# Performance work log

Measured on AMD Instinct MI355X. Metric: run time of the kernel, lower is better.

The kernel has to match this reference:

```python
import jax, jax.numpy as jnp
import numpy as np

P = 64          # num_populations
T = 8192        # buffer_size (buffer assumed full / all valid)
K = 8           # num_bins
HIST = 2        # history_length
NPAST = K ** HIST          # number of single-series past states
NCOMB = NPAST * NPAST      # joint (y_past, x_past) states
N = T - HIST - 1           # n_samples per pair


def _discretize(x):
    # Faithful to torch _discretize: min-max normalize, floor into K bins.
    xmin = x.min()
    xmax = x.max()
    rng = xmax - xmin
    norm = (x - xmin) / (rng + 1e-8)
    b = jnp.clip((norm * (K - 1)).astype(jnp.int32), 0, K - 1)
    return jnp.where(rng < 1e-8, jnp.zeros_like(b), b)


def _cond_entropy(counts, state_mask):
    # counts: (S, K) histogram of y_future per conditioning state.
    # Torch skips states with total count < 2; weight = count/N.
    tot = counts.sum(axis=1)                          # (S,)
    valid = (tot >= 2.0) & state_mask
    p = counts / jnp.maximum(tot[:, None], 1.0)
    p_safe = jnp.where(counts > 0, p, 1.0)
    h = -jnp.where(counts > 0, p * jnp.log2(p_safe), 0.0).sum(axis=1)
    w = tot / N
    return jnp.where(valid, w * h, 0.0).sum()


def _te(src_d, tgt_d):
    # src_d, tgt_d: (T,) int bins. TE(src -> tgt) in bits.
    yf = tgt_d[HIST + 1: HIST + 1 + N]                # y_future, (N,)
    # hash of k-step histories: sum_i K**i * series[k-i : k-i+N]
    yp = sum((K ** i) * tgt_d[HIST - i: HIST - i + N] for i in range(HIST))
    xp = sum((K ** i) * src_d[HIST - i: HIST - i + N] for i in range(HIST))
    # joint histograms via scatter-add (the fused histogram kernel target)
    cy = jnp.zeros((NPAST, K), jnp.float32).at[yp, yf].add(1.0)
    cc = jnp.zeros((NCOMB, K), jnp.float32).at[yp * NPAST + xp, yf].add(1.0)
    # torch loops yp in range(min(NPAST, N)) -> mask out higher state ids
    mask_y = jnp.arange(NPAST) < min(NPAST, N)
    h_y_given_yp = _cond_entropy(cy, mask_y)
    h_y_given_ypxp = _cond_entropy(cc, jnp.ones((NCOMB,), dtype=bool))
    return jnp.maximum(0.0, h_y_given_yp - h_y_given_ypxp)


def setup_inputs() -> dict:
    key = jax.random.key(0)
    return {"time_series": jax.random.normal(key, (T, P), dtype=jnp.float32)}


def reference(time_series):
    # time_series: (T, P). Returns flow_matrix (P, P): flow[i, j] = TE(i -> j).
    d = jax.vmap(_discretize, in_axes=1, out_axes=0)(time_series)  # (P, T) int
    flow = jax.vmap(lambda s: jax.vmap(lambda t: _te(s, t))(d))(d)  # (P, P)
    return flow * (1.0 - jnp.eye(P, dtype=flow.dtype))  # diagonal forced to 0
```

## Files before the change

kernel.cpp:

```cpp
#include <hip/hip_runtime.h>

static constexpr int T = 8192;
static constexpr int P = 64;
static constexpr int NSAMP = 8189;

__global__ __launch_bounds__(1024) void prep_kernel(const float* __restrict__ ts,
        unsigned short* __restrict__ A, unsigned short* __restrict__ X,
        float* __restrict__ h_y)
{
    __shared__ float col[T];
    __shared__ unsigned char bins[T];
    __shared__ unsigned int cy[512];
    __shared__ float wred[32];
    const int p = blockIdx.x, tid = threadIdx.x;
    const int lane = tid & 63, wave = tid >> 6;

    float mn = 3.402823466e38f, mx = -3.402823466e38f;
    for (int t = tid; t < T; t += 1024) {
        float v = ts[t * P + p];
        col[t] = v;
        mn = fminf(mn, v);
        mx = fmaxf(mx, v);
    }
    #pragma unroll
    for (int off = 32; off > 0; off >>= 1) {
        mn = fminf(mn, __shfl_down(mn, off, 64));
        mx = fmaxf(mx, __shfl_down(mx, off, 64));
    }
    if (lane == 0) { wred[wave] = mn; wred[16 + wave] = mx; }
    for (int i = tid; i < 512; i += 1024) cy[i] = 0u;
    __syncthreads();
    float xmin = wred[0], xmax = wred[16];
    #pragma unroll
    for (int j = 1; j < 16; ++j) {
        xmin = fminf(xmin, wred[j]);
        xmax = fmaxf(xmax, wred[16 + j]);
    }
    const float rng = xmax - xmin;
    const float den = rng + 1e-8f;
    const int flat = rng < 1e-8f;

    for (int t = tid; t < T; t += 1024) {
        float norm = (col[t] - xmin) / den;
        int b = (int)(norm * 7.0f);
        b = b < 0 ? 0 : (b > 7 ? 7 : b);
        bins[t] = flat ? (unsigned char)0 : (unsigned char)b;
    }
    __syncthreads();

    unsigned short* Ap = A + p * T;
    unsigned short* Xp = X + p * T;
    for (int i = tid * 4; i + 3 < NSAMP; i += 4096) {
        unsigned w0 = *(const unsigned*)&bins[i];
        unsigned w1 = *(const unsigned*)&bins[i + 4];
        unsigned long long bb = (unsigned long long)w0 | ((unsigned long long)w1 << 32);
        ushort4 av, xv;
        unsigned short* ap = (unsigned short*)&av;
        unsigned short* xp = (unsigned short*)&xv;
        #pragma unroll
        for (int j = 0; j < 4; ++j) {
            unsigned b1 = (unsigned)(bb >> (8 * (j + 1))) & 255u;
            unsigned b2 = (unsigned)(bb >> (8 * (j + 2))) & 255u;
            unsigned b3 = (unsigned)(bb >> (8 * (j + 3))) & 255u;
            unsigned yp = b2 + 8u * b1;
            ap[j] = (unsigned short)(yp * 512u + b3);
            xp[j] = (unsigned short)(yp * 8u);
            atomicAdd(&cy[yp * 8u + b3], 1u);
        }
        *(ushort4*)(Ap + i) = av;
        *(ushort4*)(Xp + i) = xv;
    }
    if (tid == 0) {
        unsigned b1 = bins[NSAMP], b2 = bins[NSAMP + 1], b3 = bins[NSAMP + 2];
        unsigned yp = b2 + 8u * b1;
        Ap[NSAMP - 1] = (unsigned short)(yp * 512u + b3);
        Xp[NSAMP - 1] = (unsigned short)(yp * 8u);
        atomicAdd(&cy[yp * 8u + b3], 1u);
    }
    __syncthreads();

    if (tid < 64) {
        float tot = 0.0f, sc = 0.0f;
        #pragma unroll
        for (int v = 0; v < 8; ++v) {
            unsigned c = cy[tid * 8 + v];
            if (c) { float fc = (float)c; tot += fc; sc += fc * log2f(fc); }
        }
        float acc = (tot >= 2.0f) ? (tot * log2f(tot) - sc) : 0.0f;
        #pragma unroll
        for (int off = 32; off > 0; off >>= 1) acc += __shfl_down(acc, off, 64);
        if (tid == 0) h_y[p] = acc * (1.0f / (float)NSAMP);
    }
}

__global__ __launch_bounds__(256) void pair_kernel(const unsigned short* __restrict__ A,
        const unsigned short* __restrict__ X, const float* __restrict__ h_y,
        float* __restrict__ out)
{
    const int src = blockIdx.x >> 6, tgt = blockIdx.x & 63, tid = threadIdx.x;
    if (src == tgt) { if (tid == 0) out[blockIdx.x] = 0.0f; return; }

    __shared__ unsigned int hj[8192];
    __shared__ float red[4];

    uint4* z = (uint4*)hj;
    for (int i = tid; i < 2048; i += 256) z[i] = make_uint4(0u, 0u, 0u, 0u);
    __syncthreads();

    const unsigned short* At = A + tgt * T;
    const unsigned short* Xs = X + src * T;

    auto step = [&](unsigned a, unsigned x) {
        unsigned jc = a + x;
        unsigned st = jc >> 3, yf = jc & 7u;
        unsigned scr = (st * 0x2C5u) & 4095u;
        unsigned cell = (scr << 3) | yf;
        atomicAdd(&hj[cell >> 2], 1u << ((cell & 3u) << 3));
    };

    for (int i = tid * 8; i + 7 < NSAMP; i += 2048) {
        uint4 aw = *(const uint4*)(At + i);
        uint4 xw = *(const uint4*)(Xs + i);
        step(aw.x & 0xffffu, xw.x & 0xffffu); step(aw.x >> 16, xw.x >> 16);
        step(aw.y & 0xffffu, xw.y & 0xffffu); step(aw.y >> 16, xw.y >> 16);
        step(aw.z & 0xffffu, xw.z & 0xffffu); step(aw.z >> 16, xw.z >> 16);
        step(aw.w & 0xffffu, xw.w & 0xffffu); step(aw.w >> 16, xw.w >> 16);
    }
    if (tid < 5) step(At[8184 + tid], Xs[8184 + tid]);
    __syncthreads();

    float acc = 0.0f;
    for (int s = tid; s < 4096; s += 256) {
        uint2 wv = *(const uint2*)&hj[s * 2];
        unsigned w0 = wv.x, w1 = wv.y;
        unsigned s01 = (w0 & 0x00FF00FFu) + ((w0 >> 8) & 0x00FF00FFu);
        unsigned s23 = (w1 & 0x00FF00FFu) + ((w1 >> 8) & 0x00FF00FFu);
        unsigned ss = s01 + s23;
        unsigned tot = (ss & 0xFFFFu) + (ss >> 16);
        if (tot >= 2u) {
            float sc = 0.0f;
            #pragma unroll
            for (int b = 0; b < 4; ++b) {
                float f0 = (float)((w0 >> (8 * b)) & 255u);
                float f1 = (float)((w1 >> (8 * b)) & 255u);
                sc += f0 * __log2f(fmaxf(f0, 1.0f));
                sc += f1 * __log2f(fmaxf(f1, 1.0f));
            }
            float ft = (float)tot;
            acc += ft * __log2f(ft) - sc;
        }
    }

    #pragma unroll
    for (int off = 32; off > 0; off >>= 1) acc += __shfl_down(acc, off, 64);
    if ((tid & 63) == 0) red[tid >> 6] = acc;
    __syncthreads();
    if (tid == 0) {
        float h2 = (red[0] + red[1] + red[2] + red[3]) * (1.0f / (float)NSAMP);
        out[blockIdx.x] = fmaxf(0.0f, h_y[tgt] - h2);
    }
}

extern "C" void kernel_launch(void* const* d_in, const int* in_sizes, int n_in,
                              void* d_out, int out_size, void* d_ws, size_t ws_size,
                              hipStream_t stream)
{
    const float* ts = (const float*)d_in[0];
    float* out = (float*)d_out;
    unsigned short* A = (unsigned short*)d_ws;
    unsigned short* X = A + P * T;
    float* h_y = (float*)(X + P * T);

    prep_kernel<<<dim3(P), dim3(1024), 0, stream>>>(ts, A, X, h_y);
    pair_kernel<<<dim3(P * P), dim3(256), 0, stream>>>(A, X, h_y, out);
}
```

Measured before the change: 104.1 us.

## Precompute scrambled histogram addresses in prep and compute entropy from per-sample gathers

The state scramble multiply is folded into the prep kernel using its linearity. The pair kernel then forms each cell address by adding two packed 16-bit words and masking, with no per-sample hashing. The sum of c*log2(c) is now computed by gathering each sample's own cell count and adding its log2, which replaces eight log2 calls per state with one per sample plus one per state total. This cuts transcendental work and integer ALU in the hot kernel. In exchange it keeps 16 packed addresses live in registers and adds byte gathers from shared memory after the histogram phase.

```diff
diff --git a/kernel.cpp b/kernel.cpp
--- a/kernel.cpp
+++ b/kernel.cpp
@@ -63,8 +63,8 @@
             unsigned b2 = (unsigned)(bb >> (8 * (j + 2))) & 255u;
             unsigned b3 = (unsigned)(bb >> (8 * (j + 3))) & 255u;
             unsigned yp = b2 + 8u * b1;
-            ap[j] = (unsigned short)(yp * 512u + b3);
-            xp[j] = (unsigned short)(yp * 8u);
+            ap[j] = (unsigned short)(((yp * 320u) & 4095u) * 8u + b3);
+            xp[j] = (unsigned short)(((yp * 709u) & 4095u) * 8u);
             atomicAdd(&cy[yp * 8u + b3], 1u);
         }
         *(ushort4*)(Ap + i) = av;
@@ -73,8 +73,8 @@
     if (tid == 0) {
         unsigned b1 = bins[NSAMP], b2 = bins[NSAMP + 1], b3 = bins[NSAMP + 2];
         unsigned yp = b2 + 8u * b1;
-        Ap[NSAMP - 1] = (unsigned short)(yp * 512u + b3);
-        Xp[NSAMP - 1] = (unsigned short)(yp * 8u);
+        Ap[NSAMP - 1] = (unsigned short)(((yp * 320u) & 4095u) * 8u + b3);
+        Xp[NSAMP - 1] = (unsigned short)(((yp * 709u) & 4095u) * 8u);
         atomicAdd(&cy[yp * 8u + b3], 1u);
     }
     __syncthreads();
@@ -110,46 +110,64 @@
     const unsigned short* At = A + tgt * T;
     const unsigned short* Xs = X + src * T;
 
-    auto step = [&](unsigned a, unsigned x) {
-        unsigned jc = a + x;
-        unsigned st = jc >> 3, yf = jc & 7u;
-        unsigned scr = (st * 0x2C5u) & 4095u;
-        unsigned cell = (scr << 3) | yf;
-        atomicAdd(&hj[cell >> 2], 1u << ((cell & 3u) << 3));
-    };
+    unsigned pc[16];
+    unsigned cT = 0;
 
-    for (int i = tid * 8; i + 7 < NSAMP; i += 2048) {
-        uint4 aw = *(const uint4*)(At + i);
-        uint4 xw = *(const uint4*)(Xs + i);
-        step(aw.x & 0xffffu, xw.x & 0xffffu); step(aw.x >> 16, xw.x >> 16);
-        step(aw.y & 0xffffu, xw.y & 0xffffu); step(aw.y >> 16, xw.y >> 16);
-        step(aw.z & 0xffffu, xw.z & 0xffffu); step(aw.z >> 16, xw.z >> 16);
-        step(aw.w & 0xffffu, xw.w & 0xffffu); step(aw.w >> 16, xw.w >> 16);
+    #pragma unroll
+    for (int it = 0; it < 4; ++it) {
+        const int i = tid * 8 + it * 2048;
+        if (it < 3 || tid < 255) {
+            uint4 aw = *(const uint4*)(At + i);
+            uint4 xw = *(const uint4*)(Xs + i);
+            unsigned p0 = (aw.x + xw.x) & 0x7FFF7FFFu;
+            unsigned p1 = (aw.y + xw.y) & 0x7FFF7FFFu;
+            unsigned p2 = (aw.z + xw.z) & 0x7FFF7FFFu;
+            unsigned p3 = (aw.w + xw.w) & 0x7FFF7FFFu;
+            pc[it * 4 + 0] = p0; pc[it * 4 + 1] = p1;
+            pc[it * 4 + 2] = p2; pc[it * 4 + 3] = p3;
+            atomicAdd(&hj[(p0 & 0x7FFFu) >> 2], 1u << ((p0 & 3u) << 3));
+            atomicAdd(&hj[p0 >> 18],            1u << (((p0 >> 16) & 3u) << 3));
+            atomicAdd(&hj[(p1 & 0x7FFFu) >> 2], 1u << ((p1 & 3u) << 3));
+            atomicAdd(&hj[p1 >> 18],            1u << (((p1 >> 16) & 3u) << 3));
+            atomicAdd(&hj[(p2 & 0x7FFFu) >> 2], 1u << ((p2 & 3u) << 3));
+            atomicAdd(&hj[p2 >> 18],            1u << (((p2 >> 16) & 3u) << 3));
+            atomicAdd(&hj[(p3 & 0x7FFFu) >> 2], 1u << ((p3 & 3u) << 3));
+            atomicAdd(&hj[p3 >> 18],            1u << (((p3 >> 16) & 3u) << 3));
+        }
     }
-    if (tid < 5) step(At[8184 + tid], Xs[8184 + tid]);
+    if (tid < 5) {
+        unsigned s = ((unsigned)At[8184 + tid] + (unsigned)Xs[8184 + tid]) & 0x7FFFu;
+        cT = s;
+        atomicAdd(&hj[s >> 2], 1u << ((s & 3u) << 3));
+    }
     __syncthreads();
 
+    const unsigned char* hc = (const unsigned char*)hj;
     float acc = 0.0f;
+    #pragma unroll
+    for (int it = 0; it < 4; ++it) {
+        if (it < 3 || tid < 255) {
+            #pragma unroll
+            for (int j = 0; j < 4; ++j) {
+                unsigned pcv = pc[it * 4 + j];
+                acc += __log2f((float)hc[pcv & 0xFFFFu]);
+                acc += __log2f((float)hc[pcv >> 16]);
+            }
+        }
+    }
+    if (tid < 5) acc += __log2f((float)hc[cT]);
+
+    float tpart = 0.0f;
     for (int s = tid; s < 4096; s += 256) {
         uint2 wv = *(const uint2*)&hj[s * 2];
-        unsigned w0 = wv.x, w1 = wv.y;
-        unsigned s01 = (w0 & 0x00FF00FFu) + ((w0 >> 8) & 0x00FF00FFu);
-        unsigned s23 = (w1 & 0x00FF00FFu) + ((w1 >> 8) & 0x00FF00FFu);
-        unsigned ss = s01 + s23;
+        unsigned s0 = (wv.x & 0x00FF00FFu) + ((wv.x >> 8) & 0x00FF00FFu);
+        unsigned s1 = (wv.y & 0x00FF00FFu) + ((wv.y >> 8) & 0x00FF00FFu);
+        unsigned ss = s0 + s1;
         unsigned tot = (ss & 0xFFFFu) + (ss >> 16);
-        if (tot >= 2u) {
-            float sc = 0.0f;
-            #pragma unroll
-            for (int b = 0; b < 4; ++b) {
-                float f0 = (float)((w0 >> (8 * b)) & 255u);
-                float f1 = (float)((w1 >> (8 * b)) & 255u);
-                sc += f0 * __log2f(fmaxf(f0, 1.0f));
-                sc += f1 * __log2f(fmaxf(f1, 1.0f));
-            }
-            float ft = (float)tot;
-            acc += ft * __log2f(ft) - sc;
-        }
+        float ft = (float)tot;
+        tpart += ft * __log2f(fmaxf(ft, 1.0f));
     }
+    acc = tpart - acc;
 
     #pragma unroll
     for (int off = 32; off > 0; off >>= 1) acc += __shfl_down(acc, off, 64);
```

Result: faster. 96.68 us (-7.1%).
